# Optimization experiments

Hardware: AMD Instinct MI355X
Metric: run time of the kernel (lower is better)

Reference implementation:

```python
import jax, jax.numpy as jnp
import numpy as np

N_SEQ = 250000
L = 40
C_IN = 20
K = 4
D = 32
N_BAGS = 100
SEQ_PER_BAG = N_SEQ // N_BAGS


def _param(key, shape):
    # matches torch init: normal(0, sqrt(1/prod(shape)))
    return jax.random.normal(key, shape, dtype=jnp.float32) * np.sqrt(1.0 / np.prod(shape))


def setup_inputs() -> dict:
    key = jax.random.key(0)
    ks = jax.random.split(key, 16)
    inp = {
        "x": jax.random.normal(ks[0], (N_SEQ, L, C_IN), dtype=jnp.float32),
        # equal-size bags: 100 bags of 2500 sequences (sum == N_SEQ)
        "n_per_bag": jnp.full((N_BAGS,), SEQ_PER_BAG, dtype=jnp.int32),
        # CNN: two conv1d layers, kernel shape (K, in, out) for 'NWC'/'WIO'
        "conv1_w": _param(ks[1], (K, C_IN, D)), "conv1_b": jnp.zeros((D,), jnp.float32),
        "conv2_w": _param(ks[2], (K, D, D)),    "conv2_b": jnp.zeros((D,), jnp.float32),
        # attention MLP: 32->32->32->1
        "att_w1": _param(ks[3], (D, D)), "att_b1": jnp.zeros((D,), jnp.float32),
        "att_w2": _param(ks[4], (D, D)), "att_b2": jnp.zeros((D,), jnp.float32),
        "att_w3": _param(ks[5], (D, 1)), "att_b3": jnp.zeros((1,), jnp.float32),
        # output net A: 32->32->21, output net B: 32->32->40
        "outA_w1": _param(ks[6], (D, D)),  "outA_b1": jnp.zeros((D,), jnp.float32),
        "outA_w2": _param(ks[7], (D, 21)), "outA_b2": jnp.zeros((21,), jnp.float32),
        "outB_w1": _param(ks[8], (D, D)),  "outB_b1": jnp.zeros((D,), jnp.float32),
        "outB_w2": _param(ks[9], (D, 40)), "outB_b2": jnp.zeros((40,), jnp.float32),
    }
    return inp


def _conv1d_nwc(x, w, b):
    # x: (N, L, Cin), w: (K, Cin, Cout) -> (N, L-K+1, Cout), VALID padding
    return jax.lax.conv_general_dilated(
        x, w, window_strides=(1,), padding="VALID",
        dimension_numbers=("NWC", "WIO", "NWC")) + b


def _forward(x, n_per_bag, conv1_w, conv1_b, conv2_w, conv2_b,
             att_w1, att_b1, att_w2, att_b2, att_w3, att_b3,
             outA_w1, outA_b1, outA_w2, outA_b2,
             outB_w1, outB_b1, outB_w2, outB_b2):
    selu = jax.nn.selu
    # --- sequence embedding CNN (dropout = identity in eval) ---
    h = selu(_conv1d_nwc(x, conv1_w, conv1_b))          # (N, L-3, D)
    h = selu(_conv1d_nwc(h, conv2_w, conv2_b))          # (N, L-6, D)
    seq_embed = h.max(axis=1)                           # (N, D)
    # --- attention scores ---
    a = selu(seq_embed @ att_w1 + att_b1)
    a = selu(a @ att_w2 + att_b2)
    scores = (a @ att_w3 + att_b3)[:, 0]                # (N,)
    # --- per-bag segment softmax + weighted-sum pooling ---
    seg = jnp.repeat(jnp.arange(N_BAGS, dtype=jnp.int32), np.asarray(n_per_bag),
                     total_repeat_length=seq_embed.shape[0])
    seg_max = jax.ops.segment_max(scores, seg, num_segments=N_BAGS)
    e = jnp.exp(scores - seg_max[seg])
    denom = jax.ops.segment_sum(e, seg, num_segments=N_BAGS)
    w = e / denom[seg]                                  # (N,)
    pooled = jax.ops.segment_sum(seq_embed * w[:, None], seg,
                                 num_segments=N_BAGS)   # (N_BAGS, D)
    # --- output networks (n_layers=2: one hidden SELU layer + final, then sigmoid) ---
    pa = jax.nn.sigmoid(selu(pooled @ outA_w1 + outA_b1) @ outA_w2 + outA_b2)
    pb = jax.nn.sigmoid(selu(pooled @ outB_w1 + outB_b1) @ outB_w2 + outB_b2)
    return pa, pb


def reference(x, n_per_bag, conv1_w, conv1_b, conv2_w, conv2_b,
              att_w1, att_b1, att_w2, att_b2, att_w3, att_b3,
              outA_w1, outA_b1, outA_w2, outA_b2,
              outB_w1, outB_b1, outB_w2, outB_b2):
    return _forward(x, n_per_bag, conv1_w, conv1_b, conv2_w, conv2_b,
                    att_w1, att_b1, att_w2, att_b2, att_w3, att_b3,
                    outA_w1, outA_b1, outA_w2, outA_b2,
                    outB_w1, outB_b1, outB_w2, outB_b2)
```

## Files before the change

kernel.cpp:

```cpp
#include <hip/hip_runtime.h>

#define N_SEQ 250000
#define LSEQ  40
#define CIN   20
#define KW    4
#define DCH   32
#define L1    37
#define L2    34
#define N_BAGS 100
#define SPB   2500
#define S_BLK 8
#define R1    (S_BLK * L1)
#define R2    (S_BLK * L2)
#define T1    19
#define T2    17

typedef _Float16 f16;
typedef _Float16 f16x8 __attribute__((ext_vector_type(8)));
typedef _Float16 f16x4 __attribute__((ext_vector_type(4)));
typedef float    f32x4 __attribute__((ext_vector_type(4)));

__device__ __forceinline__ float selu_f(float x) {
  float e = 1.6732632423543772f * (__expf(x) - 1.0f);
  return 1.0507009873554805f * ((x > 0.0f) ? x : e);
}

__global__ __launch_bounds__(256) void seq_kernel(
    const float* __restrict__ x,
    const float* __restrict__ w1, const float* __restrict__ b1,
    const float* __restrict__ w2, const float* __restrict__ b2,
    const float* __restrict__ aw1, const float* __restrict__ ab1,
    const float* __restrict__ aw2, const float* __restrict__ ab2,
    const float* __restrict__ aw3, const float* __restrict__ ab3,
    float* __restrict__ se_out, float* __restrict__ sc_out)
{
  __shared__ __align__(16) f16 xs[S_BLK * LSEQ * DCH];
  __shared__ __align__(16) f16 h1[S_BLK * L1 * DCH];
  __shared__ float sebuf[S_BLK * DCH];
  __shared__ float abuf[S_BLK * DCH];

  const int tid  = threadIdx.x;
  const int lane = tid & 63;
  const int wave = tid >> 6;
  const int n0   = lane & 15;
  const int quad = lane >> 4;

  const int seq0 = blockIdx.x * S_BLK;

  f16x8 bf1[KW][2], bf2[KW][2];
  #pragma unroll
  for (int t = 0; t < KW; t++) {
    #pragma unroll
    for (int j = 0; j < 8; j++) {
      const int c = quad * 8 + j;
      float v0 = 0.0f, v1 = 0.0f;
      if (c < CIN) {
        v0 = w1[(t * CIN + c) * DCH + n0];
        v1 = w1[(t * CIN + c) * DCH + n0 + 16];
      }
      bf1[t][0][j] = (f16)v0;
      bf1[t][1][j] = (f16)v1;
      bf2[t][0][j] = (f16)w2[(t * DCH + c) * DCH + n0];
      bf2[t][1][j] = (f16)w2[(t * DCH + c) * DCH + n0 + 16];
    }
  }
  const float bias1a = b1[n0], bias1b = b1[n0 + 16];
  const float bias2a = b2[n0], bias2b = b2[n0 + 16];

  {
    const f16x4 z4 = {(f16)0.f, (f16)0.f, (f16)0.f, (f16)0.f};
    for (int zi = tid; zi < S_BLK * LSEQ * 3; zi += 256) {
      const int row = zi / 3, part = zi - row * 3;
      *(f16x4*)&xs[row * DCH + CIN + part * 4] = z4;
    }
    const float4* xg = (const float4*)(x + (size_t)blockIdx.x * (S_BLK * LSEQ * CIN));
    for (int i = tid; i < S_BLK * LSEQ * CIN / 4; i += 256) {
      const float4 v = xg[i];
      const int gf = i * 4;
      const int s = gf / (LSEQ * CIN);
      const int f = gf - s * (LSEQ * CIN);
      const int l = f / CIN, c = f - l * CIN;
      f16x4 h; h[0] = (f16)v.x; h[1] = (f16)v.y; h[2] = (f16)v.z; h[3] = (f16)v.w;
      *(f16x4*)&xs[(s * LSEQ + l) * DCH + c] = h;
    }
  }
  __syncthreads();

  for (int tile = wave; tile < T1; tile += 4) {
    int r = tile * 16 + n0;
    const bool valid_a = (r < R1);
    if (!valid_a) r = 0;
    const int s = r / L1, l = r - s * L1;
    f32x4 c0 = {0.f, 0.f, 0.f, 0.f}, c1 = {0.f, 0.f, 0.f, 0.f};
    #pragma unroll
    for (int t = 0; t < KW; t++) {
      const f16x8 a = *(const f16x8*)&xs[((s * LSEQ + l + t) << 5) + (quad << 3)];
      c0 = __builtin_amdgcn_mfma_f32_16x16x32_f16(a, bf1[t][0], c0, 0, 0, 0);
      c1 = __builtin_amdgcn_mfma_f32_16x16x32_f16(a, bf1[t][1], c1, 0, 0, 0);
    }
    #pragma unroll
    for (int reg = 0; reg < 4; reg++) {
      const int rr = tile * 16 + quad * 4 + reg;
      if (rr < R1) {
        const int s2 = rr / L1, l2 = rr - s2 * L1;
        h1[((s2 * L1 + l2) << 5) + n0]      = (f16)selu_f(c0[reg] + bias1a);
        h1[((s2 * L1 + l2) << 5) + n0 + 16] = (f16)selu_f(c1[reg] + bias1b);
      }
    }
  }
  __syncthreads();

  f16* h2 = xs;
  for (int tile = wave; tile < T2; tile += 4) {
    const int r = tile * 16 + n0;
    const int s = r / L2, l = r - s * L2;
    f32x4 c0 = {0.f, 0.f, 0.f, 0.f}, c1 = {0.f, 0.f, 0.f, 0.f};
    #pragma unroll
    for (int t = 0; t < KW; t++) {
      const f16x8 a = *(const f16x8*)&h1[((s * L1 + l + t) << 5) + (quad << 3)];
      c0 = __builtin_amdgcn_mfma_f32_16x16x32_f16(a, bf2[t][0], c0, 0, 0, 0);
      c1 = __builtin_amdgcn_mfma_f32_16x16x32_f16(a, bf2[t][1], c1, 0, 0, 0);
    }
    #pragma unroll
    for (int reg = 0; reg < 4; reg++) {
      const int rr = tile * 16 + quad * 4 + reg;
      const int s2 = rr / L2, l2 = rr - s2 * L2;
      h2[((s2 * L2 + l2) << 5) + n0]      = (f16)selu_f(c0[reg] + bias2a);
      h2[((s2 * L2 + l2) << 5) + n0 + 16] = (f16)selu_f(c1[reg] + bias2b);
    }
  }
  __syncthreads();

  {
    const int s = tid >> 5, d = tid & 31;
    float m = -3.4e38f;
    for (int l = 0; l < L2; l++) m = fmaxf(m, (float)h2[((s * L2 + l) << 5) + d]);
    sebuf[tid] = m;
    se_out[(size_t)seq0 * DCH + tid] = m;
  }
  __syncthreads();

  {
    const int s = tid >> 5, d = tid & 31;
    float a = ab1[d];
    #pragma unroll
    for (int c = 0; c < DCH; c++) a = fmaf(sebuf[s * DCH + c], aw1[c * DCH + d], a);
    abuf[tid] = selu_f(a);
  }
  __syncthreads();

  {
    const int s = tid >> 5, d = tid & 31;
    float a = ab2[d];
    #pragma unroll
    for (int c = 0; c < DCH; c++) a = fmaf(abuf[s * DCH + c], aw2[c * DCH + d], a);
    a = selu_f(a);
    float p = a * aw3[d];
    #pragma unroll
    for (int off = 16; off > 0; off >>= 1) p += __shfl_xor(p, off, 32);
    if (d == 0) sc_out[seq0 + s] = p + ab3[0];
  }
}

__global__ __launch_bounds__(256) void bag_kernel(
    const float* __restrict__ se, const float* __restrict__ sc,
    const float* __restrict__ aw1, const float* __restrict__ ab1,
    const float* __restrict__ aw2, const float* __restrict__ ab2,
    const float* __restrict__ bw1, const float* __restrict__ bb1,
    const float* __restrict__ bw2, const float* __restrict__ bb2,
    float* __restrict__ out)
{
  const int bag = blockIdx.x, tid = threadIdx.x;
  const size_t base = (size_t)bag * SPB;

  __shared__ float pr[4][33];
  __shared__ float red[33];
  __shared__ float pool[DCH], hA[DCH], hB[DCH];

  float m = -3.4e38f;
  for (int i = tid; i < SPB; i += 256) m = fmaxf(m, sc[base + i]);
  #pragma unroll
  for (int off = 32; off > 0; off >>= 1) m = fmaxf(m, __shfl_xor(m, off, 64));
  if ((tid & 63) == 0) pr[tid >> 6][0] = m;
  __syncthreads();
  const float bagmax = fmaxf(fmaxf(pr[0][0], pr[1][0]), fmaxf(pr[2][0], pr[3][0]));
  __syncthreads();

  float acc[33];
  #pragma unroll
  for (int d = 0; d < 33; d++) acc[d] = 0.0f;
  for (int i = tid; i < SPB; i += 256) {
    const float e = __expf(sc[base + i] - bagmax);
    acc[32] += e;
    const float* sr = &se[(base + i) * DCH];
    #pragma unroll
    for (int d = 0; d < DCH; d++) acc[d] = fmaf(e, sr[d], acc[d]);
  }
  #pragma unroll
  for (int d = 0; d < 33; d++) {
    float v = acc[d];
    #pragma unroll
    for (int off = 32; off > 0; off >>= 1) v += __shfl_xor(v, off, 64);
    if ((tid & 63) == 0) pr[tid >> 6][d] = v;
  }
  __syncthreads();
  if (tid < 33) red[tid] = pr[0][tid] + pr[1][tid] + pr[2][tid] + pr[3][tid];
  __syncthreads();
  if (tid < DCH) pool[tid] = red[tid] / red[32];
  __syncthreads();

  if (tid < DCH) {
    float a = ab1[tid], b = bb1[tid];
    #pragma unroll
    for (int c = 0; c < DCH; c++) {
      a = fmaf(pool[c], aw1[c * DCH + tid], a);
      b = fmaf(pool[c], bw1[c * DCH + tid], b);
    }
    hA[tid] = selu_f(a);
    hB[tid] = selu_f(b);
  }
  __syncthreads();

  if (tid < 21) {
    float v = ab2[tid];
    #pragma unroll
    for (int d = 0; d < DCH; d++) v = fmaf(hA[d], aw2[d * 21 + tid], v);
    out[bag * 21 + tid] = 1.0f / (1.0f + __expf(-v));
  } else if (tid >= 32 && tid < 72) {
    const int j = tid - 32;
    float v = bb2[j];
    #pragma unroll
    for (int d = 0; d < DCH; d++) v = fmaf(hB[d], bw2[d * 40 + j], v);
    out[N_BAGS * 21 + bag * 40 + j] = 1.0f / (1.0f + __expf(-v));
  }
}

extern "C" void kernel_launch(void* const* d_in, const int* in_sizes, int n_in,
                              void* d_out, int out_size, void* d_ws, size_t ws_size,
                              hipStream_t stream)
{
  const float* x    = (const float*)d_in[0];
  const float* c1w  = (const float*)d_in[2];
  const float* c1b  = (const float*)d_in[3];
  const float* c2w  = (const float*)d_in[4];
  const float* c2b  = (const float*)d_in[5];
  const float* aw1  = (const float*)d_in[6];
  const float* ab1  = (const float*)d_in[7];
  const float* aw2  = (const float*)d_in[8];
  const float* ab2  = (const float*)d_in[9];
  const float* aw3  = (const float*)d_in[10];
  const float* ab3  = (const float*)d_in[11];
  const float* oaw1 = (const float*)d_in[12];
  const float* oab1 = (const float*)d_in[13];
  const float* oaw2 = (const float*)d_in[14];
  const float* oab2 = (const float*)d_in[15];
  const float* obw1 = (const float*)d_in[16];
  const float* obb1 = (const float*)d_in[17];
  const float* obw2 = (const float*)d_in[18];
  const float* obb2 = (const float*)d_in[19];
  float* out = (float*)d_out;

  float* se = (float*)d_ws;
  float* sc = se + (size_t)N_SEQ * DCH;

  const int nblk = N_SEQ / S_BLK;
  seq_kernel<<<nblk, 256, 0, stream>>>(x, c1w, c1b, c2w, c2b,
                                       aw1, ab1, aw2, ab2, aw3, ab3, se, sc);
  bag_kernel<<<N_BAGS, 256, 0, stream>>>(se, sc, oaw1, oab1, oaw2, oab2,
                                         obw1, obb1, obw2, obb2, out);
}
```

Before: 1.572 ms.

## Restructure conv as im2col 32x32x16 MFMA with pretransposed fp16 weights

```diff
diff --git a/kernel.cpp b/kernel.cpp
--- a/kernel.cpp
+++ b/kernel.cpp
@@ -12,148 +12,173 @@
 #define S_BLK 8
 #define R1    (S_BLK * L1)
 #define R2    (S_BLK * L2)
-#define T1    19
-#define T2    17
+#define T1C   10
+#define T2C   9
+#define H1S   36
+#define H2S   33
 
 typedef _Float16 f16;
 typedef _Float16 f16x8 __attribute__((ext_vector_type(8)));
 typedef _Float16 f16x4 __attribute__((ext_vector_type(4)));
-typedef float    f32x4 __attribute__((ext_vector_type(4)));
+typedef float    f32x16 __attribute__((ext_vector_type(16)));
 
 __device__ __forceinline__ float selu_f(float x) {
   float e = 1.6732632423543772f * (__expf(x) - 1.0f);
   return 1.0507009873554805f * ((x > 0.0f) ? x : e);
 }
 
-__global__ __launch_bounds__(256) void seq_kernel(
+__global__ __launch_bounds__(256) void prep_kernel(
+    const float* __restrict__ w1, const float* __restrict__ w2,
+    const float* __restrict__ aw1, const float* __restrict__ aw2,
+    f16* __restrict__ w1T, f16* __restrict__ w2T,
+    float* __restrict__ aw1T, float* __restrict__ aw2T)
+{
+  const int tid = threadIdx.x;
+  for (int i = tid; i < 32 * 80; i += 256) {
+    const int n = i / 80, k = i - n * 80;
+    w1T[i] = (f16)w1[k * 32 + n];
+  }
+  for (int i = tid; i < 32 * 128; i += 256) {
+    const int n = i >> 7, k = i & 127;
+    w2T[i] = (f16)w2[k * 32 + n];
+  }
+  for (int i = tid; i < 1024; i += 256) {
+    const int d = i >> 5, c = i & 31;
+    aw1T[i] = aw1[c * 32 + d];
+    aw2T[i] = aw2[c * 32 + d];
+  }
+}
+
+__global__ __launch_bounds__(256, 4) void seq_kernel(
     const float* __restrict__ x,
-    const float* __restrict__ w1, const float* __restrict__ b1,
-    const float* __restrict__ w2, const float* __restrict__ b2,
-    const float* __restrict__ aw1, const float* __restrict__ ab1,
-    const float* __restrict__ aw2, const float* __restrict__ ab2,
+    const f16*  __restrict__ w1T, const float* __restrict__ b1,
+    const f16*  __restrict__ w2T, const float* __restrict__ b2,
+    const float* __restrict__ aw1T, const float* __restrict__ ab1,
+    const float* __restrict__ aw2T, const float* __restrict__ ab2,
     const float* __restrict__ aw3, const float* __restrict__ ab3,
-    float* __restrict__ se_out, float* __restrict__ sc_out)
+    f16* __restrict__ se_out, float* __restrict__ sc_out)
 {
-  __shared__ __align__(16) f16 xs[S_BLK * LSEQ * DCH];
-  __shared__ __align__(16) f16 h1[S_BLK * L1 * DCH];
-  __shared__ float sebuf[S_BLK * DCH];
-  __shared__ float abuf[S_BLK * DCH];
+  __shared__ __align__(16) f16 reg1[R2 * H2S];
+  __shared__ __align__(16) f16 reg2[R1 * H1S];
+
+  f16* xs = reg1;
+  f16* h2 = reg1;
+  f16* h1 = reg2;
+  float* sebuf = (float*)reg2;
+  float* abuf  = sebuf + 256;
 
   const int tid  = threadIdx.x;
   const int lane = tid & 63;
   const int wave = tid >> 6;
-  const int n0   = lane & 15;
-  const int quad = lane >> 4;
-
+  const int m    = lane & 31;
+  const int half = lane >> 5;
   const int seq0 = blockIdx.x * S_BLK;
 
-  f16x8 bf1[KW][2], bf2[KW][2];
-  #pragma unroll
-  for (int t = 0; t < KW; t++) {
-    #pragma unroll
-    for (int j = 0; j < 8; j++) {
-      const int c = quad * 8 + j;
-      float v0 = 0.0f, v1 = 0.0f;
-      if (c < CIN) {
-        v0 = w1[(t * CIN + c) * DCH + n0];
-        v1 = w1[(t * CIN + c) * DCH + n0 + 16];
-      }
-      bf1[t][0][j] = (f16)v0;
-      bf1[t][1][j] = (f16)v1;
-      bf2[t][0][j] = (f16)w2[(t * DCH + c) * DCH + n0];
-      bf2[t][1][j] = (f16)w2[(t * DCH + c) * DCH + n0 + 16];
-    }
-  }
-  const float bias1a = b1[n0], bias1b = b1[n0 + 16];
-  const float bias2a = b2[n0], bias2b = b2[n0 + 16];
-
-  {
-    const f16x4 z4 = {(f16)0.f, (f16)0.f, (f16)0.f, (f16)0.f};
-    for (int zi = tid; zi < S_BLK * LSEQ * 3; zi += 256) {
-      const int row = zi / 3, part = zi - row * 3;
-      *(f16x4*)&xs[row * DCH + CIN + part * 4] = z4;
-    }
+  f16x8 bf1[5], bf2[8];
+  {
+    const f16x8* w1t8 = (const f16x8*)w1T;
+    const f16x8* w2t8 = (const f16x8*)w2T;
+    #pragma unroll
+    for (int kc = 0; kc < 5; kc++) bf1[kc] = w1t8[m * 10 + kc * 2 + half];
+    #pragma unroll
+    for (int kc = 0; kc < 8; kc++) bf2[kc] = w2t8[m * 16 + kc * 2 + half];
+  }
+  const float b1v = b1[m], b2v = b2[m];
+
+  {
     const float4* xg = (const float4*)(x + (size_t)blockIdx.x * (S_BLK * LSEQ * CIN));
     for (int i = tid; i < S_BLK * LSEQ * CIN / 4; i += 256) {
       const float4 v = xg[i];
-      const int gf = i * 4;
-      const int s = gf / (LSEQ * CIN);
-      const int f = gf - s * (LSEQ * CIN);
-      const int l = f / CIN, c = f - l * CIN;
       f16x4 h; h[0] = (f16)v.x; h[1] = (f16)v.y; h[2] = (f16)v.z; h[3] = (f16)v.w;
-      *(f16x4*)&xs[(s * LSEQ + l) * DCH + c] = h;
-    }
-  }
-  __syncthreads();
-
-  for (int tile = wave; tile < T1; tile += 4) {
-    int r = tile * 16 + n0;
-    const bool valid_a = (r < R1);
-    if (!valid_a) r = 0;
-    const int s = r / L1, l = r - s * L1;
-    f32x4 c0 = {0.f, 0.f, 0.f, 0.f}, c1 = {0.f, 0.f, 0.f, 0.f};
-    #pragma unroll
-    for (int t = 0; t < KW; t++) {
-      const f16x8 a = *(const f16x8*)&xs[((s * LSEQ + l + t) << 5) + (quad << 3)];
-      c0 = __builtin_amdgcn_mfma_f32_16x16x32_f16(a, bf1[t][0], c0, 0, 0, 0);
-      c1 = __builtin_amdgcn_mfma_f32_16x16x32_f16(a, bf1[t][1], c1, 0, 0, 0);
-    }
-    #pragma unroll
-    for (int reg = 0; reg < 4; reg++) {
-      const int rr = tile * 16 + quad * 4 + reg;
-      if (rr < R1) {
-        const int s2 = rr / L1, l2 = rr - s2 * L1;
-        h1[((s2 * L1 + l2) << 5) + n0]      = (f16)selu_f(c0[reg] + bias1a);
-        h1[((s2 * L1 + l2) << 5) + n0 + 16] = (f16)selu_f(c1[reg] + bias1b);
-      }
-    }
-  }
-  __syncthreads();
-
-  f16* h2 = xs;
-  for (int tile = wave; tile < T2; tile += 4) {
-    const int r = tile * 16 + n0;
-    const int s = r / L2, l = r - s * L2;
-    f32x4 c0 = {0.f, 0.f, 0.f, 0.f}, c1 = {0.f, 0.f, 0.f, 0.f};
-    #pragma unroll
-    for (int t = 0; t < KW; t++) {
-      const f16x8 a = *(const f16x8*)&h1[((s * L1 + l + t) << 5) + (quad << 3)];
-      c0 = __builtin_amdgcn_mfma_f32_16x16x32_f16(a, bf2[t][0], c0, 0, 0, 0);
-      c1 = __builtin_amdgcn_mfma_f32_16x16x32_f16(a, bf2[t][1], c1, 0, 0, 0);
-    }
-    #pragma unroll
-    for (int reg = 0; reg < 4; reg++) {
-      const int rr = tile * 16 + quad * 4 + reg;
-      const int s2 = rr / L2, l2 = rr - s2 * L2;
-      h2[((s2 * L2 + l2) << 5) + n0]      = (f16)selu_f(c0[reg] + bias2a);
-      h2[((s2 * L2 + l2) << 5) + n0 + 16] = (f16)selu_f(c1[reg] + bias2b);
+      *(f16x4*)&xs[i * 4] = h;
+    }
+  }
+  __syncthreads();
+
+  for (int tile = wave; tile < T1C; tile += 4) {
+    const unsigned r  = tile * 32 + m;
+    const unsigned rc = (r < R1) ? r : (R1 - 1);
+    const unsigned s  = rc / L1, l = rc - s * L1;
+    const f16* arow = &xs[(s * LSEQ + l) * CIN];
+    f32x16 acc;
+    #pragma unroll
+    for (int i = 0; i < 16; i++) acc[i] = b1v;
+    #pragma unroll
+    for (int kc = 0; kc < 5; kc++) {
+      const int e = kc * 16 + half * 8;
+      const f16x4 p0 = *(const f16x4*)(arow + e);
+      const f16x4 p1 = *(const f16x4*)(arow + e + 4);
+      const f16x8 a = __builtin_shufflevector(p0, p1, 0, 1, 2, 3, 4, 5, 6, 7);
+      acc = __builtin_amdgcn_mfma_f32_32x32x16_f16(a, bf1[kc], acc, 0, 0, 0);
+    }
+    #pragma unroll
+    for (int reg = 0; reg < 16; reg++) {
+      const int rr = tile * 32 + (reg & 3) + 8 * (reg >> 2) + 4 * half;
+      if (rr < R1) h1[rr * H1S + m] = (f16)selu_f(acc[reg]);
+    }
+  }
+  __syncthreads();
+
+  for (int tile = wave; tile < T2C; tile += 4) {
+    const unsigned r  = tile * 32 + m;
+    const unsigned rc = (r < R2) ? r : (R2 - 1);
+    const unsigned s  = rc / L2, l = rc - s * L2;
+    const f16* abase = &h1[(s * L1 + l) * H1S];
+    f32x16 acc;
+    #pragma unroll
+    for (int i = 0; i < 16; i++) acc[i] = b2v;
+    #pragma unroll
+    for (int kc = 0; kc < 8; kc++) {
+      const int e = (kc >> 1) * H1S + (kc & 1) * 16 + half * 8;
+      const f16x4 p0 = *(const f16x4*)(abase + e);
+      const f16x4 p1 = *(const f16x4*)(abase + e + 4);
+      const f16x8 a = __builtin_shufflevector(p0, p1, 0, 1, 2, 3, 4, 5, 6, 7);
+      acc = __builtin_amdgcn_mfma_f32_32x32x16_f16(a, bf2[kc], acc, 0, 0, 0);
+    }
+    #pragma unroll
+    for (int reg = 0; reg < 16; reg++) {
+      const int rr = tile * 32 + (reg & 3) + 8 * (reg >> 2) + 4 * half;
+      if (rr < R2) h2[rr * H2S + m] = (f16)acc[reg];
     }
   }
   __syncthreads();
 
   {
     const int s = tid >> 5, d = tid & 31;
-    float m = -3.4e38f;
-    for (int l = 0; l < L2; l++) m = fmaxf(m, (float)h2[((s * L2 + l) << 5) + d]);
-    sebuf[tid] = m;
-    se_out[(size_t)seq0 * DCH + tid] = m;
+    float mx = -3.4e38f;
+    for (int l = 0; l < L2; l++) mx = fmaxf(mx, (float)h2[(s * L2 + l) * H2S + d]);
+    const float sv = selu_f(mx);
+    sebuf[tid] = sv;
+    se_out[(size_t)seq0 * DCH + tid] = (f16)sv;
   }
   __syncthreads();
 
   {
     const int s = tid >> 5, d = tid & 31;
+    const float4* wt = (const float4*)aw1T;
     float a = ab1[d];
     #pragma unroll
-    for (int c = 0; c < DCH; c++) a = fmaf(sebuf[s * DCH + c], aw1[c * DCH + d], a);
+    for (int c4 = 0; c4 < 8; c4++) {
+      const float4 w = wt[d * 8 + c4];
+      const float* sb = &sebuf[s * DCH + c4 * 4];
+      a = fmaf(sb[0], w.x, a); a = fmaf(sb[1], w.y, a);
+      a = fmaf(sb[2], w.z, a); a = fmaf(sb[3], w.w, a);
+    }
     abuf[tid] = selu_f(a);
   }
   __syncthreads();
 
   {
     const int s = tid >> 5, d = tid & 31;
+    const float4* wt = (const float4*)aw2T;
     float a = ab2[d];
     #pragma unroll
-    for (int c = 0; c < DCH; c++) a = fmaf(abuf[s * DCH + c], aw2[c * DCH + d], a);
+    for (int c4 = 0; c4 < 8; c4++) {
+      const float4 w = wt[d * 8 + c4];
+      const float* sb = &abuf[s * DCH + c4 * 4];
+      a = fmaf(sb[0], w.x, a); a = fmaf(sb[1], w.y, a);
+      a = fmaf(sb[2], w.z, a); a = fmaf(sb[3], w.w, a);
+    }
     a = selu_f(a);
     float p = a * aw3[d];
     #pragma unroll
@@ -163,7 +188,7 @@
 }
 
 __global__ __launch_bounds__(256) void bag_kernel(
-    const float* __restrict__ se, const float* __restrict__ sc,
+    const f16* __restrict__ se, const float* __restrict__ sc,
     const float* __restrict__ aw1, const float* __restrict__ ab1,
     const float* __restrict__ aw2, const float* __restrict__ ab2,
     const float* __restrict__ bw1, const float* __restrict__ bb1,
@@ -192,9 +217,13 @@
   for (int i = tid; i < SPB; i += 256) {
     const float e = __expf(sc[base + i] - bagmax);
     acc[32] += e;
-    const float* sr = &se[(base + i) * DCH];
-    #pragma unroll
-    for (int d = 0; d < DCH; d++) acc[d] = fmaf(e, sr[d], acc[d]);
+    const f16* sr = &se[(base + i) * DCH];
+    #pragma unroll
+    for (int q = 0; q < 8; q++) {
+      const f16x4 v = *(const f16x4*)(sr + q * 4);
+      #pragma unroll
+      for (int j = 0; j < 4; j++) acc[q * 4 + j] = fmaf(e, (float)v[j], acc[q * 4 + j]);
+    }
   }
   #pragma unroll
   for (int d = 0; d < 33; d++) {
@@ -260,12 +289,18 @@
   const float* obb2 = (const float*)d_in[19];
   float* out = (float*)d_out;
 
-  float* se = (float*)d_ws;
-  float* sc = se + (size_t)N_SEQ * DCH;
-
-  const int nblk = N_SEQ / S_BLK;
-  seq_kernel<<<nblk, 256, 0, stream>>>(x, c1w, c1b, c2w, c2b,
-                                       aw1, ab1, aw2, ab2, aw3, ab3, se, sc);
-  bag_kernel<<<N_BAGS, 256, 0, stream>>>(se, sc, oaw1, oab1, oaw2, oab2,
+  char* ws = (char*)d_ws;
+  f16*   seh  = (f16*)ws;
+  float* sc   = (float*)(ws + (size_t)16000000);
+  f16*   w1T  = (f16*)(ws + (size_t)17000000);
+  f16*   w2T  = w1T + 2560 + 2560;
+  float* aw1T = (float*)(ws + (size_t)17000000 + 32768);
+  float* aw2T = aw1T + 1024;
+
+  prep_kernel<<<1, 256, 0, stream>>>(c1w, c2w, aw1, aw2, w1T, w2T, aw1T, aw2T);
+  seq_kernel<<<N_SEQ / S_BLK, 256, 0, stream>>>(x, w1T, c1b, w2T, c2b,
+                                                aw1T, ab1, aw2T, ab2, aw3, ab3,
+                                                seh, sc);
+  bag_kernel<<<N_BAGS, 256, 0, stream>>>(seh, sc, oaw1, oab1, oaw2, oab2,
                                          obw1, obb1, obw2, obb2, out);
 }
```

Measured after the change: 1.436 ms. -8.6%, faster.
